# Kernel optimization log

Hardware: AMD Instinct MI355X
Metric: run time of the kernel (lower is better)

Reference implementation:

```python
import jax, jax.numpy as jnp
import numpy as np

N = 128
MAX_LEN = 1024
L = 1024
BATCH = 32


def _legs_transition(n):
    # HiPPO-LegS A, B matrices (float64 numpy, matches torch module's transition())
    q = np.arange(n, dtype=np.float64)
    col, row = np.meshgrid(q, q)
    r = 2 * q + 1
    M = -(np.where(row >= col, r, 0) - np.diag(q))
    T = np.sqrt(np.diag(2 * q + 1))
    A = T @ M @ np.linalg.inv(T)
    B = np.diag(T)
    return A, B


def _stacked_bilinear(n, max_length):
    # Bilinear discretization per timestep t: (I - A/(2t))^{-1} (I + A/(2t)), (I - A/(2t))^{-1} B/t
    A, B = _legs_transition(n)
    t = np.arange(1, max_length + 1, dtype=np.float64)[:, None, None]  # (L,1,1)
    I = np.eye(n)
    At = A[None] / t                                   # (L,N,N)
    lhs = I - At / 2
    A_st = np.linalg.solve(lhs, I + At / 2)            # (L,N,N)
    Bt = (B[None, :] / t[:, 0, 0][:, None])[..., None]  # (L,N,1)
    B_st = np.linalg.solve(lhs, Bt)[..., 0]            # (L,N)
    return A_st.astype(np.float32), B_st.astype(np.float32)


def setup_inputs() -> dict:
    key = jax.random.key(0)
    inputs = jax.random.normal(key, (L, BATCH), dtype=jnp.float32)
    A_st, B_st = _stacked_bilinear(N, MAX_LEN)
    return {
        "inputs": inputs,
        "A_stacked": jnp.asarray(A_st),
        "B_stacked": jnp.asarray(B_st),
    }


def reference(inputs, A_stacked, B_stacked):
    # inputs: (L, B); A_stacked: (L, N, N); B_stacked: (L, N)
    Lc = inputs.shape[0]
    u = inputs[..., None] * B_stacked[:Lc, None, :]  # (L, B, N)

    def step(s, Au):
        A_t, u_t = Au                                 # (N,N), (B,N)
        s = jnp.einsum("ij,bj->bi", A_t, s) + u_t
        return s, s

    s0 = jnp.zeros_like(u[0])
    _, xs = jax.lax.scan(step, s0, (A_stacked[:Lc], u))
    return xs  # (L, B, N)
```

## Files before the change

kernel.cpp:

```cpp
#include <hip/hip_runtime.h>


#define LDK 136
#define PKF 11264

using f16 = _Float16;
typedef __attribute__((ext_vector_type(8))) f16 f16x8;
typedef __attribute__((ext_vector_type(4))) f16 f16x4;
typedef __attribute__((ext_vector_type(4))) float f32x4;

__device__ __forceinline__ f32x4 mfma3(f16x8 ah, f16x8 al, f16x8 bh, f16x8 bl,
                                       f32x4 c) {
  c = __builtin_amdgcn_mfma_f32_16x16x32_f16(ah, bh, c, 0, 0, 0);
  c = __builtin_amdgcn_mfma_f32_16x16x32_f16(ah, bl, c, 0, 0, 0);
  c = __builtin_amdgcn_mfma_f32_16x16x32_f16(al, bh, c, 0, 0, 0);
  return c;
}

__device__ __forceinline__ void split8(const float* v, f16x8& h, f16x8& l) {
#pragma unroll
  for (int j = 0; j < 8; ++j) {
    const float x = v[j];
    const f16 hh = (f16)x;
    h[j] = hh;
    l[j] = (f16)(x - (float)hh);
  }
}

__device__ __forceinline__ int slot2mt(int h, int slot) {
  if (h == 0) return (slot & 1) ? 7 - (slot >> 1) : (slot >> 1);
  return (slot & 1) ? 5 - (slot >> 1) : 2 + (slot >> 1);
}

__device__ __forceinline__ void gload_lds16(const float* g, float* l) {
  __builtin_amdgcn_global_load_lds(
      (const __attribute__((address_space(1))) unsigned int*)g,
      (__attribute__((address_space(3))) unsigned int*)l, 16, 0, 0);
}


__device__ __forceinline__ int pk_src_off(int m) {
  int b, local, ccm1, sh;
  if (m < 128)      { b = 0; local = m;       ccm1 = 3;  sh = 2; }
  else if (m < 384) { b = 1; local = m - 128; ccm1 = 7;  sh = 3; }
  else if (m < 896) { b = 2; local = m - 384; ccm1 = 15; sh = 4; }
  else              { b = 3; local = m - 896; ccm1 = 15; sh = 4; }
  const int ri = local >> sh, cp = local & ccm1;
  const int c = cp ^ (ri & ccm1);
  return (b * 32 + ri) * 128 + c * 8;
}

__device__ __forceinline__ void read_pk(const f16* __restrict__ Bs, int nt,
                                        int lr, int j0, f16x8& v) {
  const int b = nt >> 1;
  const int ri = ((nt & 1) << 4) + lr;
  const int ccm1 = (b == 0) ? 3 : (b == 1) ? 7 : 15;
  const int fb = (b == 0) ? 0 : (b == 1) ? 1024 : (b == 2) ? 3072 : 7168;
  const int c = j0 ^ (ri & ccm1);
  v = *(const f16x8*)(Bs + fb + ri * ((ccm1 + 1) * 8) + c * 8);
}

template <int NT, int IT>
__device__ __forceinline__ void pk_precompute(int tid, int (&src)[IT]) {
#pragma unroll
  for (int it = 0; it < IT; ++it) {
    const int m = tid + it * NT;
    src[it] = (m < 1408) ? pk_src_off(m) : 0;
  }
}

template <int NT, int IT>
__device__ __forceinline__ void pk_stage(const f16* __restrict__ gMh,
                                         const f16* __restrict__ gMl,
                                         f16* __restrict__ dH,
                                         f16* __restrict__ dL,
                                         const int (&src)[IT], int tid) {
#pragma unroll
  for (int it = 0; it < IT; ++it) {
    const int m = tid + it * NT;
    if (m < 1408) {
      gload_lds16((const float*)(gMh + src[it]), (float*)(dH + m * 8));
      gload_lds16((const float*)(gMl + src[it]), (float*)(dL + m * 8));
    }
  }
}

__device__ __forceinline__ void compute_soff(int tid, int (&soff)[8]) {
#pragma unroll
  for (int it = 0; it < 8; ++it) {
    const int m = tid + it * 320;
    if (m < 2304) {
      const int kt = (m >= 768) + (m >= 1536) + (m >= 2048);
      const int local = m - ((kt >= 1) * 768 + (kt >= 2) * 768 + (kt >= 3) * 512);
      const int rp = local >> 3, c = local & 7;
      const int r = rp + 32 + (kt >= 2) * 32 + (kt >= 3) * 32;
      soff[it] = r * 128 + kt * 32 + ((c ^ (rp & 7)) << 2);
    } else {
      soff[it] = 0;
    }
  }
}

__device__ __forceinline__ void issue_A(const float* __restrict__ Al,
                                        float* __restrict__ Ast,
                                        const int (&soff)[8], int tid) {
#pragma unroll
  for (int it = 0; it < 8; ++it) {
    if (it < 7 || tid < 64)
      gload_lds16(Al + soff[it], Ast + (tid + it * 320) * 4);
  }
}

__device__ __forceinline__ void read_staged(const float* __restrict__ Ast,
                                            int nt, int kt, int lr, int q,
                                            f16x8& ch, f16x8& cl) {
  const int rp = nt * 16 + lr - (32 + (kt >= 2) * 32 + (kt >= 3) * 32);
  const float* pb =
      Ast + ((kt >= 1) * 3072 + (kt >= 2) * 3072 + (kt >= 3) * 2048) + rp * 32;
  float raw[8];
  *(float4*)&raw[0] = *(const float4*)(pb + (((2 * q + 0) ^ (rp & 7)) << 2));
  *(float4*)&raw[4] = *(const float4*)(pb + (((2 * q + 1) ^ (rp & 7)) << 2));
  split8(raw, ch, cl);
}

__device__ __forceinline__ void chain_step_k1(const float* __restrict__ Acur,
                                              const float* __restrict__ Anext,
                                              const float* __restrict__ x32,
                                              const float* __restrict__ Bvl,
                                              f16* __restrict__ Ph,
                                              f16* __restrict__ Pl,
                                              float* __restrict__ Ast,
                                              const int (&soff)[8],
                                              int wv, int mt) {
  const int tid = threadIdx.x;
  const int lane = tid & 63, lr = lane & 15, q = lane >> 4;
  const bool wrow = (mt >= 8);
  const int ktA0 = wrow ? 0 : (mt >> 1);
  f16x8 ah[4], al[4];
#pragma unroll
  for (int kt = 0; kt < 4; ++kt) {
    if (kt >= ktA0) {
      const int off = (wv * 16 + lr) * LDK + kt * 32 + q * 8;
      ah[kt] = *(const f16x8*)(Ph + off);
      al[kt] = *(const f16x8*)(Pl + off);
    }
  }
  const bool need0 = wrow || mt == 0;
  const bool need1 = wrow || mt <= 1;
  float dir0[8], dir1[8];
  if (need0) {
    const float* p = Acur + lr * 128 + q * 8;
    *(float4*)&dir0[0] = *(const float4*)p;
    *(float4*)&dir0[4] = *(const float4*)(p + 4);
  }
  if (need1) {
    const float* p = Acur + (16 + lr) * 128 + q * 8;
    *(float4*)&dir1[0] = *(const float4*)p;
    *(float4*)&dir1[4] = *(const float4*)(p + 4);
  }
  f32x4 acc[8];
#pragma unroll
  for (int nt = 0; nt < 8; ++nt) acc[nt] = (f32x4){0.f, 0.f, 0.f, 0.f};
#pragma unroll
  for (int nt = 2; nt < 8; ++nt) {
    if (wrow || nt >= mt) {
#pragma unroll
      for (int kt = 0; kt < 4; ++kt) {
        if (kt >= ktA0 && kt <= (nt >> 1)) {
          f16x8 ch, cl;
          read_staged(Ast, nt, kt, lr, q, ch, cl);
          acc[nt] = mfma3(ah[kt], al[kt], ch, cl, acc[nt]);
        }
      }
    }
  }
  if (need0) {
    f16x8 ch, cl;
    split8(dir0, ch, cl);
    acc[0] = mfma3(ah[0], al[0], ch, cl, acc[0]);
  }
  if (need1) {
    f16x8 ch, cl;
    split8(dir1, ch, cl);
    acc[1] = mfma3(ah[0], al[0], ch, cl, acc[1]);
  }
  __syncthreads();
  if (Anext) issue_A(Anext, Ast, soff, tid);
#pragma unroll
  for (int nt = 0; nt < 8; ++nt) {
    if (!(wrow || nt >= mt)) continue;
    float v[4] = {acc[nt][0], acc[nt][1], acc[nt][2], acc[nt][3]};
    if (wrow) {
      const int b0 = (mt - 8) * 16 + q * 4;
      const float4 x4 = *(const float4*)(x32 + b0);
      const float bn = Bvl[nt * 16 + lr];
      v[0] += bn * x4.x; v[1] += bn * x4.y; v[2] += bn * x4.z; v[3] += bn * x4.w;
    }
#pragma unroll
    for (int r = 0; r < 4; ++r) {
      const int o = (wv * 16 + q * 4 + r) * LDK + nt * 16 + lr;
      const f16 hh = (f16)v[r];
      Ph[o] = hh;
      Pl[o] = (f16)(v[r] - (float)hh);
    }
  }
  __syncthreads();
}

__device__ __forceinline__ void chain_copyout(const f16* __restrict__ Ph,
                                              const f16* __restrict__ Pl, int h,
                                              f16* __restrict__ oMh,
                                              f16* __restrict__ oMl,
                                              float* __restrict__ oW) {
  const int tid = threadIdx.x;
  for (int t = tid; t < 1024; t += 320) {
    const int i = t >> 3;
    const int slot = (t >> 1) & 3;
    const int half = t & 1;
    const int mtg = slot2mt(h, slot);
    const int y0 = mtg * 16 + half * 8;
    if ((y0 >> 5) > (i >> 5)) continue;
    f16x8 hv, lv;
#pragma unroll
    for (int e = 0; e < 8; ++e) {
      hv[e] = Ph[(slot * 16 + half * 8 + e) * LDK + i];
      lv[e] = Pl[(slot * 16 + half * 8 + e) * LDK + i];
    }
    *(f16x8*)(oMh + i * 128 + y0) = hv;
    *(f16x8*)(oMl + i * 128 + y0) = lv;
  }
  for (int t = tid; t < 512; t += 320) {
    const int n = t >> 2, b4 = (t & 3) * 4;
    float4 o;
    float* po = (float*)&o;
#pragma unroll
    for (int e = 0; e < 4; ++e)
      po[e] = (float)Ph[(64 + b4 + e) * LDK + n] + (float)Pl[(64 + b4 + e) * LDK + n];
    *(float4*)(oW + n * 32 + h * 16 + b4) = o;
  }
}

__device__ __forceinline__ void state_step_h_b16(const f16* __restrict__ Bh16,
                                                 const f16* __restrict__ Bl16,
                                                 const float* __restrict__ aux0,
                                                 f16* __restrict__ Sh,
                                                 f16* __restrict__ Sl, int h) {
  const int tid = threadIdx.x;
  const int wv4 = tid >> 6;
  const bool act = (wv4 < 4);
  const int wv = wv4 & 3;
  const int lane = tid & 63, lr = lane & 15, q = lane >> 4;
  const int nts[2] = {wv, 7 - wv};
  const int ktAmax = (7 - wv) >> 1;
  f16x8 ah[4], al[4];
  f16x8 bh[2][4], bl[2][4];
  f32x4 acc[2];
  if (act) {
#pragma unroll
    for (int kt = 0; kt < 4; ++kt)
      if (kt <= ktAmax) {
        const int off = lr * LDK + kt * 32 + q * 8;
        ah[kt] = *(const f16x8*)(Sh + off);
        al[kt] = *(const f16x8*)(Sl + off);
      }
#pragma unroll
    for (int ni = 0; ni < 2; ++ni) {
      const int nt = nts[ni];
#pragma unroll
      for (int kt = 0; kt < 4; ++kt)
        if (kt <= (nt >> 1)) {
          const int o = (nt * 16 + lr) * 128 + kt * 32 + q * 8;
          bh[ni][kt] = *(const f16x8*)(Bh16 + o);
          bl[ni][kt] = *(const f16x8*)(Bl16 + o);
        }
    }
#pragma unroll
    for (int ni = 0; ni < 2; ++ni) acc[ni] = (f32x4){0.f, 0.f, 0.f, 0.f};
#pragma unroll
    for (int ni = 0; ni < 2; ++ni) {
      const int nt = nts[ni];
#pragma unroll
      for (int kt = 0; kt < 4; ++kt)
        if (kt <= (nt >> 1))
          acc[ni] = mfma3(ah[kt], al[kt], bh[ni][kt], bl[ni][kt], acc[ni]);
    }
  }
  __syncthreads();
  if (act) {
#pragma unroll
    for (int ni = 0; ni < 2; ++ni) {
      const int nt = nts[ni];
      float v[4] = {acc[ni][0], acc[ni][1], acc[ni][2], acc[ni][3]};
      const int bq = q * 4;
      const float4 w4 = *(const float4*)(aux0 + (nt * 16 + lr) * 32 + h * 16 + bq);
      v[0] += w4.x; v[1] += w4.y; v[2] += w4.z; v[3] += w4.w;
#pragma unroll
      for (int r = 0; r < 4; ++r) {
        const int o = (bq + r) * LDK + nt * 16 + lr;
        const f16 hh = (f16)v[r];
        Sh[o] = hh;
        Sl[o] = (f16)(v[r] - (float)hh);
      }
    }
  }
  __syncthreads();
}

__device__ __forceinline__ void state_step_h_staged(
    const float* __restrict__ Acur, const float* __restrict__ Anext,
    const float* __restrict__ x32, const float* __restrict__ Bvl,
    f16* __restrict__ Sh, f16* __restrict__ Sl, float* __restrict__ outp,
    int h, float* __restrict__ Ast, const int (&soff)[8]) {
  const int tid = threadIdx.x;
  const int wv4 = tid >> 6;
  const bool act = (wv4 < 4);
  const int wv = wv4 & 3;
  const int lane = tid & 63, lr = lane & 15, q = lane >> 4;
  const int ntL = wv, ntH = 7 - wv;
  f32x4 accL = (f32x4){0.f, 0.f, 0.f, 0.f}, accH = accL;
  if (act) {
    const int ktAmax = ntH >> 1;
    f16x8 ah[4], al[4];
#pragma unroll
    for (int kt = 0; kt < 4; ++kt)
      if (kt <= ktAmax) {
        const int off = lr * LDK + kt * 32 + q * 8;
        ah[kt] = *(const f16x8*)(Sh + off);
        al[kt] = *(const f16x8*)(Sl + off);
      }
    float dir[8];
    if (wv < 2) {
      const float* p = Acur + (ntL * 16 + lr) * 128 + q * 8;
      *(float4*)&dir[0] = *(const float4*)p;
      *(float4*)&dir[4] = *(const float4*)(p + 4);
    }
#pragma unroll
    for (int kt = 0; kt < 4; ++kt) {
      if (kt <= (ntH >> 1)) {
        f16x8 ch, cl;
        read_staged(Ast, ntH, kt, lr, q, ch, cl);
        accH = mfma3(ah[kt], al[kt], ch, cl, accH);
      }
    }
    if (wv >= 2) {
#pragma unroll
      for (int kt = 0; kt < 4; ++kt) {
        if (kt <= (ntL >> 1)) {
          f16x8 ch, cl;
          read_staged(Ast, ntL, kt, lr, q, ch, cl);
          accL = mfma3(ah[kt], al[kt], ch, cl, accL);
        }
      }
    } else {
      f16x8 ch, cl;
      split8(dir, ch, cl);
      accL = mfma3(ah[0], al[0], ch, cl, accL);
    }
  }
  __syncthreads();
  if (Anext) issue_A(Anext, Ast, soff, tid);
  if (act) {
#pragma unroll
    for (int ni = 0; ni < 2; ++ni) {
      const int nt = (ni == 0) ? ntL : ntH;
      const f32x4 a = (ni == 0) ? accL : accH;
      float v[4] = {a[0], a[1], a[2], a[3]};
      const int bq = q * 4;
      const float4 x4 = *(const float4*)(x32 + h * 16 + bq);
      const float bn = Bvl[nt * 16 + lr];
      v[0] += bn * x4.x; v[1] += bn * x4.y; v[2] += bn * x4.z; v[3] += bn * x4.w;
      if (outp) {
#pragma unroll
        for (int r = 0; r < 4; ++r)
          outp[(h * 16 + bq + r) * 128 + nt * 16 + lr] = v[r];
      }
#pragma unroll
      for (int r = 0; r < 4; ++r) {
        const int o = (bq + r) * LDK + nt * 16 + lr;
        const f16 hh = (f16)v[r];
        Sh[o] = hh;
        Sl[o] = (f16)(v[r] - (float)hh);
      }
    }
  }
  __syncthreads();
}

__global__ __launch_bounds__(320) void k1_chunks(const float* __restrict__ A,
                                                 const float* __restrict__ x,
                                                 const float* __restrict__ Bv,
                                                 f16* __restrict__ Mh,
                                                 f16* __restrict__ Ml,
                                                 float* __restrict__ Wf) {
  __shared__ f16 Ph[80 * LDK], Pl[80 * LDK];
  __shared__ float Ast[9216];
  const int tid = threadIdx.x;
  const int c = blockIdx.x >> 1, h = blockIdx.x & 1;
  const int l0 = 4 * c;
  int soff[8];
  compute_soff(tid, soff);
  issue_A(A + (size_t)(l0 + 1) * 16384, Ast, soff, tid);
  const float* A0 = A + (size_t)l0 * 16384;
  for (int t = tid; t < 2048; t += 320) {
    const int k = t >> 4, u = t & 15;
    const int slot = u >> 2, fo = (u & 3) * 4;
    const int mtg = slot2mt(h, slot);
    const int y = mtg * 16 + fo;
    float vv[4];
    if ((y >> 5) <= (k >> 5)) {
      const float4 v = *(const float4*)(A0 + k * 128 + y);
      vv[0] = v.x; vv[1] = v.y; vv[2] = v.z; vv[3] = v.w;
    } else {
      vv[0] = vv[1] = vv[2] = vv[3] = 0.f;
    }
#pragma unroll
    for (int e = 0; e < 4; ++e) {
      const f16 hh = (f16)vv[e];
      Ph[(slot * 16 + fo + e) * LDK + k] = hh;
      Pl[(slot * 16 + fo + e) * LDK + k] = (f16)(vv[e] - (float)hh);
    }
  }
  for (int t = tid; t < 512; t += 320) {
    const int b = t >> 5, n4 = (t & 31) * 4;
    const float xb = x[l0 * 32 + h * 16 + b];
#pragma unroll
    for (int e = 0; e < 4; ++e) {
      const float u = xb * Bv[l0 * 128 + n4 + e];
      const f16 hh = (f16)u;
      Ph[(64 + b) * LDK + n4 + e] = hh;
      Pl[(64 + b) * LDK + n4 + e] = (f16)(u - (float)hh);
    }
  }
  __syncthreads();
  const int wv = tid >> 6;
  const int mt = (wv == 4) ? (8 + h) : slot2mt(h, wv);
  chain_step_k1(A + (size_t)(l0 + 1) * 16384, A + (size_t)(l0 + 2) * 16384,
                x + (l0 + 1) * 32, Bv + (l0 + 1) * 128, Ph, Pl, Ast, soff, wv, mt);
  chain_step_k1(A + (size_t)(l0 + 2) * 16384, A + (size_t)(l0 + 3) * 16384,
                x + (l0 + 2) * 32, Bv + (l0 + 2) * 128, Ph, Pl, Ast, soff, wv, mt);
  chain_step_k1(A + (size_t)(l0 + 3) * 16384, nullptr,
                x + (l0 + 3) * 32, Bv + (l0 + 3) * 128, Ph, Pl, Ast, soff, wv, mt);
  chain_copyout(Ph, Pl, h, Mh + (size_t)c * 16384, Ml + (size_t)c * 16384,
                Wf + (size_t)c * 4096);
}

__global__ __launch_bounds__(192) void mscan_s(const f16* __restrict__ MhA,
                                               const f16* __restrict__ MlA,
                                               const float* __restrict__ WA,
                                               f16* __restrict__ MhB,
                                               f16* __restrict__ MlB,
                                               float* __restrict__ WB) {
  __shared__ f16 Ph[48 * LDK], Pl[48 * LDK];
  __shared__ f16 BstH[2][PKF], BstL[2][PKF];
  const int bid = blockIdx.x;
  const int g = bid & 15, unit = bid >> 4;
  const int h = unit >> 1, half = unit & 1;
  const int tid = threadIdx.x;
  const int wv = tid >> 6;
  const int lane = tid & 63, lr = lane & 15, q = lane >> 4;
  const bool isW = (half == 0 && wv == 2);
  const bool isM = (wv < 2);
  const int mt = isW ? (8 + h) : (isM ? slot2mt(h, half * 2 + wv) : 0);
  const int lw = wv * 16;
  const int ktA0 = isW ? 0 : (mt >> 1);
  const size_t n0 = (size_t)(16 * g);

  int src[8];
  pk_precompute<192, 8>(tid, src);
  pk_stage<192, 8>(MhA + (n0 + 1) * 16384, MlA + (n0 + 1) * 16384,
                   BstH[1], BstL[1], src, tid);
  if (isM) {
    const f16* pMh = MhA + n0 * 16384;
    const f16* pMl = MlA + n0 * 16384;
#pragma unroll
    for (int it = 0; it < 4; ++it) {
      const int t = lane + it * 64;
      const int k = t >> 1, hk = t & 1;
      const int y0 = mt * 16 + hk * 8;
      f16x8 hv, lv;
      if ((y0 >> 5) <= (k >> 5)) {
        hv = *(const f16x8*)(pMh + k * 128 + y0);
        lv = *(const f16x8*)(pMl + k * 128 + y0);
      } else {
#pragma unroll
        for (int e = 0; e < 8; ++e) { hv[e] = (f16)0.f; lv[e] = (f16)0.f; }
      }
#pragma unroll
      for (int e = 0; e < 8; ++e) {
        Ph[(lw + hk * 8 + e) * LDK + k] = hv[e];
        Pl[(lw + hk * 8 + e) * LDK + k] = lv[e];
      }
    }
  } else if (isW) {
    const float* pW = WA + n0 * 4096;
#pragma unroll
    for (int it = 0; it < 8; ++it) {
      const int t = lane + it * 64;
      const int n = t >> 2, b4 = (t & 3) * 4;
      const float4 w4 = *(const float4*)(pW + n * 32 + h * 16 + b4);
      const float vv[4] = {w4.x, w4.y, w4.z, w4.w};
#pragma unroll
      for (int r = 0; r < 4; ++r) {
        const f16 hh = (f16)vv[r];
        Ph[(lw + b4 + r) * LDK + n] = hh;
        Pl[(lw + b4 + r) * LDK + n] = (f16)(vv[r] - (float)hh);
      }
    }
  }
  __syncthreads();

#pragma unroll 1
  for (int j = 1; j <= 15; ++j) {
    const size_t nd = n0 + j;
    const int cur = j & 1;
    if (j < 15)
      pk_stage<192, 8>(MhA + (nd + 1) * 16384, MlA + (nd + 1) * 16384,
                       BstH[cur ^ 1], BstL[cur ^ 1], src, tid);
    float4 w4s[8];
    if (isW) {
      const float* Wn = WA + nd * 4096;
#pragma unroll
      for (int nt = 0; nt < 8; ++nt)
        w4s[nt] = *(const float4*)(Wn + (nt * 16 + lr) * 32 + h * 16 + q * 4);
    }
    f16x8 ah[4], al[4];
    if (isM || isW) {
#pragma unroll
      for (int kt = 0; kt < 4; ++kt)
        if (kt >= ktA0) {
          const int off = (lw + lr) * LDK + kt * 32 + q * 8;
          ah[kt] = *(const f16x8*)(Ph + off);
          al[kt] = *(const f16x8*)(Pl + off);
        }
    }
    f32x4 acc[8];
#pragma unroll
    for (int nt = 0; nt < 8; ++nt) acc[nt] = (f32x4){0.f, 0.f, 0.f, 0.f};
    if (isM || isW) {
      const int ntF = isW ? 0 : mt;
#pragma unroll
      for (int nt = 0; nt < 8; ++nt) {
        if (nt >= ntF) {
#pragma unroll
          for (int kt = 0; kt < 4; ++kt) {
            if (kt >= ktA0 && kt <= (nt >> 1)) {
              f16x8 bh, bl;
              const int j0 = kt * 4 + q;
              read_pk(BstH[cur], nt, lr, j0, bh);
              read_pk(BstL[cur], nt, lr, j0, bl);
              acc[nt] = mfma3(ah[kt], al[kt], bh, bl, acc[nt]);
            }
          }
        }
      }
    }
    if (isM) {
      f16* oMh = MhB + nd * 16384;
      f16* oMl = MlB + nd * 16384;
      if (mt & 1) {
        const int k = (mt - 1) * 16 + lr;
        const f16x4 z = {(f16)0.f, (f16)0.f, (f16)0.f, (f16)0.f};
        *(f16x4*)(oMh + k * 128 + mt * 16 + q * 4) = z;
        *(f16x4*)(oMl + k * 128 + mt * 16 + q * 4) = z;
      }
#pragma unroll
      for (int nt = 0; nt < 8; ++nt) {
        if (nt < mt) continue;
        f16x4 hv4, lv4;
#pragma unroll
        for (int r = 0; r < 4; ++r) {
          const float v = acc[nt][r];
          const f16 hh = (f16)v;
          const f16 ll = (f16)(v - (float)hh);
          hv4[r] = hh;
          lv4[r] = ll;
          Ph[(lw + q * 4 + r) * LDK + nt * 16 + lr] = hh;
          Pl[(lw + q * 4 + r) * LDK + nt * 16 + lr] = ll;
        }
        const int k = nt * 16 + lr;
        *(f16x4*)(oMh + k * 128 + mt * 16 + q * 4) = hv4;
        *(f16x4*)(oMl + k * 128 + mt * 16 + q * 4) = lv4;
      }
    } else if (isW) {
      float* oW = WB + nd * 4096;
#pragma unroll
      for (int nt = 0; nt < 8; ++nt) {
        float v[4];
#pragma unroll
        for (int r = 0; r < 4; ++r) v[r] = acc[nt][r];
        v[0] += w4s[nt].x; v[1] += w4s[nt].y; v[2] += w4s[nt].z; v[3] += w4s[nt].w;
#pragma unroll
        for (int r = 0; r < 4; ++r) {
          const f16 hh = (f16)v[r];
          Ph[(lw + q * 4 + r) * LDK + nt * 16 + lr] = hh;
          Pl[(lw + q * 4 + r) * LDK + nt * 16 + lr] = (f16)(v[r] - (float)hh);
        }
        const float4 o = {v[0], v[1], v[2], v[3]};
        *(float4*)(oW + (nt * 16 + lr) * 32 + h * 16 + q * 4) = o;
      }
    }
    __syncthreads();
  }
}

__global__ __launch_bounds__(256) void gscan(const f16* __restrict__ MhB,
                                             const f16* __restrict__ MlB,
                                             const float* __restrict__ WB,
                                             float* __restrict__ Ef) {
  __shared__ f16 Sh[16 * LDK], Sl[16 * LDK];
  __shared__ f16 GstH[2][PKF], GstL[2][PKF];
  const int g = blockIdx.x & 15, h = blockIdx.x >> 4;
  const int tid = threadIdx.x;
  int src[6];
  pk_precompute<256, 6>(tid, src);
  for (int t = tid; t < 16 * LDK; t += 256) { Sh[t] = (f16)0.f; Sl[t] = (f16)0.f; }
  if (g > 0)
    pk_stage<256, 6>(MhB + (size_t)15 * 16384, MlB + (size_t)15 * 16384,
                     GstH[0], GstL[0], src, tid);
  __syncthreads();
  const int wv = (tid >> 6) & 3;
  const int lane = tid & 63, lr = lane & 15, q = lane >> 4;
  const int nts[2] = {wv, 7 - wv};
  const int ktAmax = (7 - wv) >> 1;
#pragma unroll 1
  for (int t = 0; t < g; ++t) {
    const size_t nd = (size_t)(16 * t + 15);
    const int cur = t & 1;
    if (t + 1 < g) {
      const size_t nn = (size_t)(16 * (t + 1) + 15);
      pk_stage<256, 6>(MhB + nn * 16384, MlB + nn * 16384,
                       GstH[cur ^ 1], GstL[cur ^ 1], src, tid);
    }
    const float* aux0 = WB + nd * 4096;
    float4 w4s[2];
#pragma unroll
    for (int ni = 0; ni < 2; ++ni)
      w4s[ni] = *(const float4*)(aux0 + (nts[ni] * 16 + lr) * 32 + h * 16 + q * 4);
    f16x8 ah[4], al[4];
#pragma unroll
    for (int kt = 0; kt < 4; ++kt)
      if (kt <= ktAmax) {
        const int off = lr * LDK + kt * 32 + q * 8;
        ah[kt] = *(const f16x8*)(Sh + off);
        al[kt] = *(const f16x8*)(Sl + off);
      }
    f32x4 acc[2];
#pragma unroll
    for (int ni = 0; ni < 2; ++ni) acc[ni] = (f32x4){0.f, 0.f, 0.f, 0.f};
#pragma unroll
    for (int ni = 0; ni < 2; ++ni) {
      const int nt = nts[ni];
#pragma unroll
      for (int kt = 0; kt < 4; ++kt)
        if (kt <= (nt >> 1)) {
          f16x8 bh, bl;
          const int j0 = kt * 4 + q;
          read_pk(GstH[cur], nt, lr, j0, bh);
          read_pk(GstL[cur], nt, lr, j0, bl);
          acc[ni] = mfma3(ah[kt], al[kt], bh, bl, acc[ni]);
        }
    }
    __syncthreads();
#pragma unroll
    for (int ni = 0; ni < 2; ++ni) {
      const int nt = nts[ni];
      float v[4] = {acc[ni][0], acc[ni][1], acc[ni][2], acc[ni][3]};
      v[0] += w4s[ni].x; v[1] += w4s[ni].y; v[2] += w4s[ni].z; v[3] += w4s[ni].w;
#pragma unroll
      for (int r = 0; r < 4; ++r) {
        const int o = (q * 4 + r) * LDK + nt * 16 + lr;
        const f16 hh = (f16)v[r];
        Sh[o] = hh;
        Sl[o] = (f16)(v[r] - (float)hh);
      }
    }
    __syncthreads();
  }
  for (int t = tid; t < 2048; t += 256) {
    const int row = t & 15, n = t >> 4;
    Ef[(size_t)g * 4096 + n * 32 + h * 16 + row] =
        (float)Sh[row * LDK + n] + (float)Sl[row * LDK + n];
  }
}

__global__ __launch_bounds__(320) void k3h(const float* __restrict__ A,
                                           const float* __restrict__ x,
                                           const float* __restrict__ Bv,
                                           const f16* __restrict__ MhA,
                                           const f16* __restrict__ MlA,
                                           const float* __restrict__ WA,
                                           const f16* __restrict__ MhB,
                                           const f16* __restrict__ MlB,
                                           const float* __restrict__ WB,
                                           const float* __restrict__ Ef,
                                           float* __restrict__ out) {
  __shared__ f16 Sh[16 * LDK], Sl[16 * LDK];
  __shared__ float Ast[9216];
  const int tid = threadIdx.x;
  const int c = blockIdx.x >> 1, h = blockIdx.x & 1;
  const int g = c >> 4, j = c & 15;
  int soff[8];
  compute_soff(tid, soff);
  issue_A(A + (size_t)(4 * c) * 16384, Ast, soff, tid);
  const float* Ew = Ef + (size_t)g * 4096;
  for (int tt = tid; tt < 2048; tt += 320) {
    const int row = tt & 15, n = tt >> 4;
    const float v = Ew[n * 32 + h * 16 + row];
    const f16 hh = (f16)v;
    Sh[row * LDK + n] = hh;
    Sl[row * LDK + n] = (f16)(v - (float)hh);
  }
  __syncthreads();
  if (j > 0) {
    const int nd = c - 1, jp = j - 1;
    const bool inA = (jp == 0);
    const f16* mh = (inA ? MhA : MhB) + (size_t)nd * 16384;
    const f16* ml = (inA ? MlA : MlB) + (size_t)nd * 16384;
    const float* w = (inA ? WA : WB) + (size_t)nd * 4096;
    state_step_h_b16(mh, ml, w, Sh, Sl, h);
  }
#pragma unroll 1
  for (int t4 = 0; t4 < 4; ++t4) {
    const int l = 4 * c + t4;
    const float* Anext = (t4 < 3) ? A + (size_t)(l + 1) * 16384 : nullptr;
    state_step_h_staged(A + (size_t)l * 16384, Anext, x + l * 32, Bv + l * 128,
                        Sh, Sl, out + (size_t)l * 4096, h, Ast, soff);
  }
}

extern "C" void kernel_launch(void* const* d_in, const int* in_sizes, int n_in,
                              void* d_out, int out_size, void* d_ws, size_t ws_size,
                              hipStream_t stream) {
  const float* x  = (const float*)d_in[0];
  const float* A  = (const float*)d_in[1];
  const float* Bv = (const float*)d_in[2];
  float* out = (float*)d_out;

  f16* MhA = (f16*)d_ws;
  f16* MlA = MhA + 256 * 16384;
  float* WA = (float*)(MlA + 256 * 16384);
  f16* MhB = (f16*)(WA + 256 * 4096);
  f16* MlB = MhB + 256 * 16384;
  float* WB = (float*)(MlB + 256 * 16384);
  float* Ef = WB + 256 * 4096;

  k1_chunks<<<512, 320, 0, stream>>>(A, x, Bv, MhA, MlA, WA);
  mscan_s<<<64, 192, 0, stream>>>(MhA, MlA, WA, MhB, MlB, WB);
  gscan<<<32, 256, 0, stream>>>(MhB, MlB, WB, Ef);
  k3h<<<512, 320, 0, stream>>>(A, x, Bv, MhA, MlA, WA, MhB, MlB, WB, Ef, out);
}
```

Measured before the change: 249.6 us.

## Double-buffer staged A in LDS and replace syncthreads with non-draining barriers

The LDS staging buffer for the next timestep's A matrix is doubled, so the async global-to-LDS load for step t+1 is issued at the start of step t and overlaps the MFMA work, rather than waiting until after compute. The x and B operand loads are hoisted before a single vmcnt(0) wait, and __syncthreads is replaced with an lgkmcnt-only barrier so outstanding global loads are not drained. This adds LDS usage (two 36KB buffers), which may lower occupancy, and the correctness of the hand-written waitcnt logic depends on the explicit vmcnt wait at step start.

```diff
diff --git a/kernel.cpp b/kernel.cpp
--- a/kernel.cpp
+++ b/kernel.cpp
@@ -38,6 +38,17 @@
       (__attribute__((address_space(3))) unsigned int*)l, 16, 0, 0);
 }
 
+__device__ __forceinline__ void bar_nodrain() {
+  __builtin_amdgcn_sched_barrier(0);
+  asm volatile("s_waitcnt lgkmcnt(0)" ::: "memory");
+  __builtin_amdgcn_s_barrier();
+  __builtin_amdgcn_sched_barrier(0);
+}
+__device__ __forceinline__ void wait_vm0() {
+  __builtin_amdgcn_sched_barrier(0);
+  asm volatile("s_waitcnt vmcnt(0)" ::: "memory");
+  __builtin_amdgcn_sched_barrier(0);
+}
 
 __device__ __forceinline__ int pk_src_off(int m) {
   int b, local, ccm1, sh;
@@ -123,15 +134,16 @@
   split8(raw, ch, cl);
 }
 
-__device__ __forceinline__ void chain_step_k1(const float* __restrict__ Acur,
-                                              const float* __restrict__ Anext,
-                                              const float* __restrict__ x32,
-                                              const float* __restrict__ Bvl,
-                                              f16* __restrict__ Ph,
-                                              f16* __restrict__ Pl,
-                                              float* __restrict__ Ast,
-                                              const int (&soff)[8],
-                                              int wv, int mt) {
+__device__ __forceinline__ void chain_step_k1a(const float* __restrict__ Acur,
+                                               const float* __restrict__ Anext,
+                                               const float* __restrict__ x32,
+                                               const float* __restrict__ Bvl,
+                                               f16* __restrict__ Ph,
+                                               f16* __restrict__ Pl,
+                                               const float* __restrict__ AstCur,
+                                               float* __restrict__ AstNxt,
+                                               const int (&soff)[8],
+                                               int wv, int mt) {
   const int tid = threadIdx.x;
   const int lane = tid & 63, lr = lane & 15, q = lane >> 4;
   const bool wrow = (mt >= 8);
@@ -158,6 +170,17 @@
     *(float4*)&dir1[0] = *(const float4*)p;
     *(float4*)&dir1[4] = *(const float4*)(p + 4);
   }
+  float4 x4v = {0.f, 0.f, 0.f, 0.f};
+  float bnv[8];
+  if (wrow) {
+    const int b0 = (mt - 8) * 16 + q * 4;
+    x4v = *(const float4*)(x32 + b0);
+#pragma unroll
+    for (int nt = 0; nt < 8; ++nt) bnv[nt] = Bvl[nt * 16 + lr];
+  }
+  wait_vm0();
+  bar_nodrain();
+  if (Anext) issue_A(Anext, AstNxt, soff, tid);
   f32x4 acc[8];
 #pragma unroll
   for (int nt = 0; nt < 8; ++nt) acc[nt] = (f32x4){0.f, 0.f, 0.f, 0.f};
@@ -168,7 +191,7 @@
       for (int kt = 0; kt < 4; ++kt) {
         if (kt >= ktA0 && kt <= (nt >> 1)) {
           f16x8 ch, cl;
-          read_staged(Ast, nt, kt, lr, q, ch, cl);
+          read_staged(AstCur, nt, kt, lr, q, ch, cl);
           acc[nt] = mfma3(ah[kt], al[kt], ch, cl, acc[nt]);
         }
       }
@@ -184,17 +207,13 @@
     split8(dir1, ch, cl);
     acc[1] = mfma3(ah[0], al[0], ch, cl, acc[1]);
   }
-  __syncthreads();
-  if (Anext) issue_A(Anext, Ast, soff, tid);
 #pragma unroll
   for (int nt = 0; nt < 8; ++nt) {
     if (!(wrow || nt >= mt)) continue;
     float v[4] = {acc[nt][0], acc[nt][1], acc[nt][2], acc[nt][3]};
     if (wrow) {
-      const int b0 = (mt - 8) * 16 + q * 4;
-      const float4 x4 = *(const float4*)(x32 + b0);
-      const float bn = Bvl[nt * 16 + lr];
-      v[0] += bn * x4.x; v[1] += bn * x4.y; v[2] += bn * x4.z; v[3] += bn * x4.w;
+      v[0] += bnv[nt] * x4v.x; v[1] += bnv[nt] * x4v.y;
+      v[2] += bnv[nt] * x4v.z; v[3] += bnv[nt] * x4v.w;
     }
 #pragma unroll
     for (int r = 0; r < 4; ++r) {
@@ -204,7 +223,7 @@
       Pl[o] = (f16)(v[r] - (float)hh);
     }
   }
-  __syncthreads();
+  bar_nodrain();
 }
 
 __device__ __forceinline__ void chain_copyout(const f16* __restrict__ Ph,
@@ -306,21 +325,24 @@
   __syncthreads();
 }
 
-__device__ __forceinline__ void state_step_h_staged(
+__device__ __forceinline__ void state_step_h_stagedA(
     const float* __restrict__ Acur, const float* __restrict__ Anext,
     const float* __restrict__ x32, const float* __restrict__ Bvl,
     f16* __restrict__ Sh, f16* __restrict__ Sl, float* __restrict__ outp,
-    int h, float* __restrict__ Ast, const int (&soff)[8]) {
+    int h, const float* __restrict__ AstCur, float* __restrict__ AstNxt,
+    const int (&soff)[8]) {
   const int tid = threadIdx.x;
   const int wv4 = tid >> 6;
   const bool act = (wv4 < 4);
   const int wv = wv4 & 3;
   const int lane = tid & 63, lr = lane & 15, q = lane >> 4;
   const int ntL = wv, ntH = 7 - wv;
-  f32x4 accL = (f32x4){0.f, 0.f, 0.f, 0.f}, accH = accL;
+  f16x8 ah[4], al[4];
+  float dir[8];
+  float4 x4v = {0.f, 0.f, 0.f, 0.f};
+  float bnL = 0.f, bnH = 0.f;
   if (act) {
     const int ktAmax = ntH >> 1;
-    f16x8 ah[4], al[4];
 #pragma unroll
     for (int kt = 0; kt < 4; ++kt)
       if (kt <= ktAmax) {
@@ -328,17 +350,25 @@
         ah[kt] = *(const f16x8*)(Sh + off);
         al[kt] = *(const f16x8*)(Sl + off);
       }
-    float dir[8];
     if (wv < 2) {
       const float* p = Acur + (ntL * 16 + lr) * 128 + q * 8;
       *(float4*)&dir[0] = *(const float4*)p;
       *(float4*)&dir[4] = *(const float4*)(p + 4);
     }
+    x4v = *(const float4*)(x32 + h * 16 + q * 4);
+    bnL = Bvl[ntL * 16 + lr];
+    bnH = Bvl[ntH * 16 + lr];
+  }
+  wait_vm0();
+  bar_nodrain();
+  if (Anext) issue_A(Anext, AstNxt, soff, tid);
+  f32x4 accL = (f32x4){0.f, 0.f, 0.f, 0.f}, accH = accL;
+  if (act) {
 #pragma unroll
     for (int kt = 0; kt < 4; ++kt) {
       if (kt <= (ntH >> 1)) {
         f16x8 ch, cl;
-        read_staged(Ast, ntH, kt, lr, q, ch, cl);
+        read_staged(AstCur, ntH, kt, lr, q, ch, cl);
         accH = mfma3(ah[kt], al[kt], ch, cl, accH);
       }
     }
@@ -347,7 +377,7 @@
       for (int kt = 0; kt < 4; ++kt) {
         if (kt <= (ntL >> 1)) {
           f16x8 ch, cl;
-          read_staged(Ast, ntL, kt, lr, q, ch, cl);
+          read_staged(AstCur, ntL, kt, lr, q, ch, cl);
           accL = mfma3(ah[kt], al[kt], ch, cl, accL);
         }
       }
@@ -357,18 +387,16 @@
       accL = mfma3(ah[0], al[0], ch, cl, accL);
     }
   }
-  __syncthreads();
-  if (Anext) issue_A(Anext, Ast, soff, tid);
   if (act) {
 #pragma unroll
     for (int ni = 0; ni < 2; ++ni) {
       const int nt = (ni == 0) ? ntL : ntH;
+      const float bn = (ni == 0) ? bnL : bnH;
       const f32x4 a = (ni == 0) ? accL : accH;
       float v[4] = {a[0], a[1], a[2], a[3]};
       const int bq = q * 4;
-      const float4 x4 = *(const float4*)(x32 + h * 16 + bq);
-      const float bn = Bvl[nt * 16 + lr];
-      v[0] += bn * x4.x; v[1] += bn * x4.y; v[2] += bn * x4.z; v[3] += bn * x4.w;
+      v[0] += bn * x4v.x; v[1] += bn * x4v.y;
+      v[2] += bn * x4v.z; v[3] += bn * x4v.w;
       if (outp) {
 #pragma unroll
         for (int r = 0; r < 4; ++r)
@@ -383,7 +411,7 @@
       }
     }
   }
-  __syncthreads();
+  bar_nodrain();
 }
 
 __global__ __launch_bounds__(320) void k1_chunks(const float* __restrict__ A,
@@ -393,13 +421,13 @@
                                                  f16* __restrict__ Ml,
                                                  float* __restrict__ Wf) {
   __shared__ f16 Ph[80 * LDK], Pl[80 * LDK];
-  __shared__ float Ast[9216];
+  __shared__ float Ast[2][9216];
   const int tid = threadIdx.x;
   const int c = blockIdx.x >> 1, h = blockIdx.x & 1;
   const int l0 = 4 * c;
   int soff[8];
   compute_soff(tid, soff);
-  issue_A(A + (size_t)(l0 + 1) * 16384, Ast, soff, tid);
+  issue_A(A + (size_t)(l0 + 1) * 16384, Ast[1], soff, tid);
   const float* A0 = A + (size_t)l0 * 16384;
   for (int t = tid; t < 2048; t += 320) {
     const int k = t >> 4, u = t & 15;
@@ -431,15 +459,18 @@
       Pl[(64 + b) * LDK + n4 + e] = (f16)(u - (float)hh);
     }
   }
-  __syncthreads();
+  bar_nodrain();
   const int wv = tid >> 6;
   const int mt = (wv == 4) ? (8 + h) : slot2mt(h, wv);
-  chain_step_k1(A + (size_t)(l0 + 1) * 16384, A + (size_t)(l0 + 2) * 16384,
-                x + (l0 + 1) * 32, Bv + (l0 + 1) * 128, Ph, Pl, Ast, soff, wv, mt);
-  chain_step_k1(A + (size_t)(l0 + 2) * 16384, A + (size_t)(l0 + 3) * 16384,
-                x + (l0 + 2) * 32, Bv + (l0 + 2) * 128, Ph, Pl, Ast, soff, wv, mt);
-  chain_step_k1(A + (size_t)(l0 + 3) * 16384, nullptr,
-                x + (l0 + 3) * 32, Bv + (l0 + 3) * 128, Ph, Pl, Ast, soff, wv, mt);
+  chain_step_k1a(A + (size_t)(l0 + 1) * 16384, A + (size_t)(l0 + 2) * 16384,
+                 x + (l0 + 1) * 32, Bv + (l0 + 1) * 128, Ph, Pl,
+                 Ast[1], Ast[0], soff, wv, mt);
+  chain_step_k1a(A + (size_t)(l0 + 2) * 16384, A + (size_t)(l0 + 3) * 16384,
+                 x + (l0 + 2) * 32, Bv + (l0 + 2) * 128, Ph, Pl,
+                 Ast[0], Ast[1], soff, wv, mt);
+  chain_step_k1a(A + (size_t)(l0 + 3) * 16384, nullptr,
+                 x + (l0 + 3) * 32, Bv + (l0 + 3) * 128, Ph, Pl,
+                 Ast[1], Ast[0], soff, wv, mt);
   chain_copyout(Ph, Pl, h, Mh + (size_t)c * 16384, Ml + (size_t)c * 16384,
                 Wf + (size_t)c * 4096);
 }
@@ -695,13 +726,13 @@
                                            const float* __restrict__ Ef,
                                            float* __restrict__ out) {
   __shared__ f16 Sh[16 * LDK], Sl[16 * LDK];
-  __shared__ float Ast[9216];
+  __shared__ float Ast[2][9216];
   const int tid = threadIdx.x;
   const int c = blockIdx.x >> 1, h = blockIdx.x & 1;
   const int g = c >> 4, j = c & 15;
   int soff[8];
   compute_soff(tid, soff);
-  issue_A(A + (size_t)(4 * c) * 16384, Ast, soff, tid);
+  issue_A(A + (size_t)(4 * c) * 16384, Ast[0], soff, tid);
   const float* Ew = Ef + (size_t)g * 4096;
   for (int tt = tid; tt < 2048; tt += 320) {
     const int row = tt & 15, n = tt >> 4;
@@ -710,7 +741,7 @@
     Sh[row * LDK + n] = hh;
     Sl[row * LDK + n] = (f16)(v - (float)hh);
   }
-  __syncthreads();
+  bar_nodrain();
   if (j > 0) {
     const int nd = c - 1, jp = j - 1;
     const bool inA = (jp == 0);
@@ -723,8 +754,9 @@
   for (int t4 = 0; t4 < 4; ++t4) {
     const int l = 4 * c + t4;
     const float* Anext = (t4 < 3) ? A + (size_t)(l + 1) * 16384 : nullptr;
-    state_step_h_staged(A + (size_t)l * 16384, Anext, x + l * 32, Bv + l * 128,
-                        Sh, Sl, out + (size_t)l * 4096, h, Ast, soff);
+    state_step_h_stagedA(A + (size_t)l * 16384, Anext, x + l * 32,
+                         Bv + l * 128, Sh, Sl, out + (size_t)l * 4096, h,
+                         Ast[t4 & 1], (float*)Ast[(t4 + 1) & 1], soff);
   }
 }
 
```

Result: no change. 250.8 us (+0.5%).
